# Optimization experiments

Hardware: AMD Instinct MI355X
Metric: run time of the kernel (lower is better)

## Reference

```python
import jax, jax.numpy as jnp
import numpy as np
import math

B, S, D, H, F, L, V = 16, 256, 1024, 16, 4096, 6, 32
HD = D // H
EPS = 1e-6
DIST_DECAY = 0.05  # grid-distance attention decay strength
NEG = -1e9


def _ln(x, w, b):
    mu = jnp.mean(x, axis=-1, keepdims=True)
    var = jnp.mean(jnp.square(x - mu), axis=-1, keepdims=True)
    return (x - mu) * jax.lax.rsqrt(var + EPS) * w + b


def _branch_bias():
    # branch 0: grid-distance decay (distance_matrix = |i-j|)
    # branch 1: register-flow edges i<->i+1 (chain mask)
    # branch 2: entanglement edges on even pairs (2k, 2k+1)
    # branch 3: semantic (full attention, no bias)
    i = jnp.arange(S)
    dist = jnp.abs(i[:, None] - i[None, :]).astype(jnp.float32)  # [S,S]
    reg = dist <= 1.0
    ent = (i[:, None] // 2) == (i[None, :] // 2)
    bias = jnp.stack([
        -DIST_DECAY * dist,
        jnp.where(reg, 0.0, NEG),
        jnp.where(ent, 0.0, NEG),
        jnp.zeros((S, S), jnp.float32),
    ])  # [4,S,S]
    return bias[:, None, None]  # [4,1,1,S,S]


def setup_inputs() -> dict:
    key = jax.random.key(0)
    ks = jax.random.split(key, 20)
    sd = 0.02
    inp = {
        'x': jax.random.normal(ks[0], (B, S, D), jnp.float32),
        't_emb': jax.random.normal(ks[1], (B, D), jnp.float32),
        'ln1_w': jnp.ones((L, D)), 'ln1_b': jnp.zeros((L, D)),
        'ln2_w': jnp.ones((L, D)), 'ln2_b': jnp.zeros((L, D)),
        'Wqkv': jax.random.normal(ks[2], (L, 4, D, 3 * D)) * sd,
        'Wo':   jax.random.normal(ks[3], (L, 4, D, D)) * sd,
        'Wf':   jax.random.normal(ks[4], (L, 4 * D, D)) * sd,
        'bf':   jnp.zeros((L, D)),
        'W1':   jax.random.normal(ks[5], (L, D, F)) * sd,
        'W3':   jax.random.normal(ks[6], (L, D, F)) * sd,
        'W2':   jax.random.normal(ks[7], (L, F, D)) * sd,
        'Wa':   jax.random.normal(ks[8], (L, D, 6 * D)) * sd,
        'ba':   jnp.zeros((L, 6 * D)),
        'fn_w': jnp.ones((D,)), 'fn_b': jnp.zeros((D,)),
        'Wp':   jax.random.normal(ks[9], (D, V)) * sd,
        'bp':   jnp.zeros((V,)),
    }
    return inp


def _quantum_attention(xn, Wqkv_l, Wo_l, Wf_l, bf_l, bias):
    # four attention branches computed in one batched einsum over branch axis x
    qkv = jnp.einsum('bsd,xde->xbse', xn, Wqkv_l)            # [4,B,S,3D]
    qkv = qkv.reshape(4, B, S, 3, H, HD)
    q, k, v = (jnp.moveaxis(qkv[:, :, :, j], 3, 2) for j in range(3))  # [4,B,H,S,HD]
    scores = jnp.einsum('xbhsd,xbhtd->xbhst', q, k) / math.sqrt(HD) + bias
    attn = jax.nn.softmax(scores, axis=-1)
    ctx = jnp.einsum('xbhst,xbhtd->xbhsd', attn, v)          # [4,B,H,S,HD]
    ctx = jnp.moveaxis(ctx, 2, 3).reshape(4, B, S, D)
    outs = jnp.einsum('xbsd,xde->xbse', ctx, Wo_l)           # [4,B,S,D]
    cat = jnp.moveaxis(outs, 0, 2).reshape(B, S, 4 * D)
    return cat @ Wf_l + bf_l                                  # fusion network


def reference(x, t_emb, ln1_w, ln1_b, ln2_w, ln2_b, Wqkv, Wo, Wf, bf, W1, W3, W2, Wa, ba, fn_w, fn_b, Wp, bp):
    bias = _branch_bias()
    for l in range(L):
        # AdaLN timestep conditioning: SiLU -> Linear -> chunk(6)
        a = jax.nn.silu(t_emb) @ Wa[l] + ba[l]
        sh_msa, sc_msa, g_msa, sh_mlp, sc_mlp, g_mlp = jnp.split(a, 6, axis=-1)
        xn = _ln(x, ln1_w[l], ln1_b[l])
        xn = xn * (1.0 + sc_msa[:, None]) + sh_msa[:, None]
        attn_out = _quantum_attention(xn, Wqkv[l], Wo[l], Wf[l], bf[l], bias)
        x = x + g_msa[:, None] * attn_out
        xn = _ln(x, ln2_w[l], ln2_b[l])
        xn = xn * (1.0 + sc_mlp[:, None]) + sh_mlp[:, None]
        ffn = (jax.nn.silu(xn @ W1[l]) * (xn @ W3[l])) @ W2[l]  # SwiGLU
        x = x + g_mlp[:, None] * ffn
    x = _ln(x, fn_w, fn_b)
    return x @ Wp + bp  # noise predictor logits [B,S,V]
```

## Files before the change

kernel.cpp:

```cpp
#include <hip/hip_runtime.h>
#include <hip/hip_bf16.h>
#include <math.h>

#define BB 16
#define SS 256
#define DD 1024
#define HH 16
#define HDD 64
#define FF 4096
#define LL 6
#define VV 32
#define MM (BB*SS)

using bf16 = __hip_bfloat16;
using short8 = __attribute__((ext_vector_type(8))) short;
using f32x4  = __attribute__((ext_vector_type(4))) float;

__device__ __forceinline__ float bf2f(short u){
  unsigned int x = ((unsigned int)(unsigned short)u) << 16;
  return __builtin_bit_cast(float, x);
}
__device__ __forceinline__ short f2bf(float f){
  return __builtin_bit_cast(short, __float2bfloat16(f));
}

__device__ __forceinline__ void gll16(const void* g, void* l) {
  __builtin_amdgcn_global_load_lds(
      (const __attribute__((address_space(1))) void*)g,
      (__attribute__((address_space(3))) void*)l,
      16, 0, 0);
}

__device__ __forceinline__ f32x4 mfma16(short8 a, short8 b, f32x4 c){
  return __builtin_amdgcn_mfma_f32_16x16x32_bf16(a, b, c, 0, 0, 0);
}

__device__ __forceinline__ void st_out(float* p, float v){ *p = v; }
__device__ __forceinline__ void st_out(bf16* p, float v){ *p = __float2bfloat16(v); }

__global__ __launch_bounds__(256)
void tcvt64(const float* __restrict__ in, bf16* __restrict__ out,
            int R, int C, long izs, long ozs)
{
  in  += (long)blockIdx.z * izs;
  out += (long)blockIdx.z * ozs;
  __shared__ float tl[64][65];
  int c0 = blockIdx.x * 64, r0 = blockIdx.y * 64;
  int t = threadIdx.x;
  int tr = t >> 4, tc = (t & 15) * 4;
  #pragma unroll
  for (int i = 0; i < 4; ++i) {
    f32x4 v = *(const f32x4*)(in + (long)(r0 + tr + i*16) * C + c0 + tc);
    tl[tr + i*16][tc+0] = v[0];
    tl[tr + i*16][tc+1] = v[1];
    tl[tr + i*16][tc+2] = v[2];
    tl[tr + i*16][tc+3] = v[3];
  }
  __syncthreads();
  int oc = t >> 2, rch = (t & 3) * 16;
  short8 o0, o1;
  #pragma unroll
  for (int j = 0; j < 8; ++j) o0[j] = f2bf(tl[rch + j][oc]);
  #pragma unroll
  for (int j = 0; j < 8; ++j) o1[j] = f2bf(tl[rch + 8 + j][oc]);
  *(short8*)(out + (long)(c0 + oc) * R + r0 + rch)     = o0;
  *(short8*)(out + (long)(c0 + oc) * R + r0 + rch + 8) = o1;
}

__global__ __launch_bounds__(256)
void tcvt64_w13(const float* __restrict__ W1, const float* __restrict__ W3,
                bf16* __restrict__ out, long loff)
{
  const float* in = (blockIdx.z ? W3 : W1) + loff;
  const int zoff = blockIdx.z ? 16 : 0;
  __shared__ float tl[64][65];
  int c0 = blockIdx.x * 64, r0 = blockIdx.y * 64;
  int t = threadIdx.x;
  int tr = t >> 4, tc = (t & 15) * 4;
  #pragma unroll
  for (int i = 0; i < 4; ++i) {
    f32x4 v = *(const f32x4*)(in + (long)(r0 + tr + i*16) * 4096 + c0 + tc);
    tl[tr + i*16][tc+0] = v[0];
    tl[tr + i*16][tc+1] = v[1];
    tl[tr + i*16][tc+2] = v[2];
    tl[tr + i*16][tc+3] = v[3];
  }
  __syncthreads();
  int oc = t >> 2, rch = (t & 3) * 16;
  short8 o0, o1;
  #pragma unroll
  for (int j = 0; j < 8; ++j) o0[j] = f2bf(tl[rch + j][oc]);
  #pragma unroll
  for (int j = 0; j < 8; ++j) o1[j] = f2bf(tl[rch + 8 + j][oc]);
  int n = c0 + oc;
  int orow = ((n >> 4) << 5) + zoff + (n & 15);
  *(short8*)(out + (long)orow * 1024 + r0 + rch)     = o0;
  *(short8*)(out + (long)orow * 1024 + r0 + rch + 8) = o1;
}

__global__ __launch_bounds__(256)
void cvt(const float* __restrict__ in, bf16* __restrict__ out)
{
  long base = ((long)blockIdx.x * 256 + threadIdx.x) * 8;
  f32x4 a = *(const f32x4*)(in + base);
  f32x4 b = *(const f32x4*)(in + base + 4);
  short8 o;
  #pragma unroll
  for (int j = 0; j < 4; ++j) { o[j] = f2bf(a[j]); o[4+j] = f2bf(b[j]); }
  *(short8*)(out + base) = o;
}

template<typename OUT, int MODE>
__global__ __launch_bounds__(512, 2)
void gemm256(const bf16* __restrict__ A, const bf16* __restrict__ Bt,
             OUT* __restrict__ C, int K,
             int lda, int ldb, int ldc, long kzs, long czs, int swz)
{
  __shared__ short lds[65536];
  char* L = (char*)lds;
  A  += (long)blockIdx.z * kzs;
  Bt += (long)blockIdx.z * kzs;
  C  += (long)blockIdx.z * czs;
  int lin = blockIdx.x + gridDim.x * blockIdx.y;
  if (swz) {
    int nwg = gridDim.x * gridDim.y;
    int q = nwg >> 3, r = nwg & 7;
    int xcd = lin & 7, o = lin >> 3;
    lin = (xcd < r ? xcd*(q+1) : r*(q+1) + (xcd-r)*q) + o;
  }
  const int n0 = (lin % gridDim.x) * 256;
  const int m0 = (lin / gridDim.x) * 256;
  const int t = threadIdx.x;
  const int wid = t >> 6, lane = t & 63, lo = lane & 15, hi = lane >> 4;
  const int wr = wid >> 2, wc = wid & 3;
  const int rst = t >> 3;
  const int glog = (t & 7) ^ (rst & 7);
  const int wub = wid * 1024;
  const bf16* Ap = A + (long)m0 * lda + glog * 8;
  const bf16* Bp = Bt + (long)n0 * ldb + glog * 8;
  f32x4 acc[8][4] = {};
  const int nkt = K >> 6;

  auto STAGE = [&](int kt, int p, int d) {
    const long ko = (long)kt * 64;
    char* base = L + d*65536;
    if (p < 2) {
      gll16(Ap + (long)((p*2  )*64 + rst)*lda + ko, base + (p*2  )*8192 + wub);
      gll16(Ap + (long)((p*2+1)*64 + rst)*lda + ko, base + (p*2+1)*8192 + wub);
    } else {
      int pp = p - 2;
      gll16(Bp + (long)((pp*2  )*64 + rst)*ldb + ko, base + 32768 + (pp*2  )*8192 + wub);
      gll16(Bp + (long)((pp*2+1)*64 + rst)*ldb + ko, base + 32768 + (pp*2+1)*8192 + wub);
    }
  };

  #pragma unroll
  for (int p = 0; p < 4; ++p) STAGE(0, p, 0);

  short8 af[4][2], b0[2][2], b1[2][2];
  const int gk0 = ((0*4 + hi) ^ (lo & 7)) << 4;
  const int gk1 = ((1*4 + hi) ^ (lo & 7)) << 4;

  for (int kt = 0; kt < nkt; ++kt) {
    const int d = kt & 1;
    const int ktn = (kt+1 < nkt) ? kt+1 : kt;
    char* Ab = L + d*65536;
    char* Bb = Ab + 32768;
    STAGE(ktn, 0, d^1);
    __builtin_amdgcn_sched_barrier(0);
    asm volatile("s_waitcnt vmcnt(2)" ::: "memory");
    __builtin_amdgcn_sched_barrier(0);
    __builtin_amdgcn_s_barrier();
    __builtin_amdgcn_sched_barrier(0);
    #pragma unroll
    for (int mi = 0; mi < 4; ++mi) {
      int r = wr*128 + mi*16 + lo;
      af[mi][0] = *(const short8*)(Ab + r*128 + gk0);
      af[mi][1] = *(const short8*)(Ab + r*128 + gk1);
    }
    #pragma unroll
    for (int ni = 0; ni < 2; ++ni) {
      int r = wc*64 + ni*16 + lo;
      b0[ni][0] = *(const short8*)(Bb + r*128 + gk0);
      b0[ni][1] = *(const short8*)(Bb + r*128 + gk1);
    }
    __builtin_amdgcn_s_barrier();
    __builtin_amdgcn_s_setprio(1);
    #pragma unroll
    for (int mi = 0; mi < 4; ++mi)
      #pragma unroll
      for (int ni = 0; ni < 2; ++ni) {
        acc[mi][ni] = mfma16(af[mi][0], b0[ni][0], acc[mi][ni]);
        acc[mi][ni] = mfma16(af[mi][1], b0[ni][1], acc[mi][ni]);
      }
    __builtin_amdgcn_s_setprio(0);
    __builtin_amdgcn_sched_barrier(0);
    __builtin_amdgcn_s_barrier();
    STAGE(ktn, 1, d^1);
    #pragma unroll
    for (int ni = 0; ni < 2; ++ni) {
      int r = wc*64 + (2+ni)*16 + lo;
      b1[ni][0] = *(const short8*)(Bb + r*128 + gk0);
      b1[ni][1] = *(const short8*)(Bb + r*128 + gk1);
    }
    __builtin_amdgcn_s_barrier();
    __builtin_amdgcn_s_setprio(1);
    #pragma unroll
    for (int mi = 0; mi < 4; ++mi)
      #pragma unroll
      for (int ni = 0; ni < 2; ++ni) {
        acc[mi][2+ni] = mfma16(af[mi][0], b1[ni][0], acc[mi][2+ni]);
        acc[mi][2+ni] = mfma16(af[mi][1], b1[ni][1], acc[mi][2+ni]);
      }
    __builtin_amdgcn_s_setprio(0);
    __builtin_amdgcn_sched_barrier(0);
    __builtin_amdgcn_s_barrier();
    STAGE(ktn, 2, d^1);
    #pragma unroll
    for (int mi = 0; mi < 4; ++mi) {
      int r = wr*128 + (4+mi)*16 + lo;
      af[mi][0] = *(const short8*)(Ab + r*128 + gk0);
      af[mi][1] = *(const short8*)(Ab + r*128 + gk1);
    }
    __builtin_amdgcn_s_barrier();
    __builtin_amdgcn_s_setprio(1);
    #pragma unroll
    for (int mi = 0; mi < 4; ++mi)
      #pragma unroll
      for (int ni = 0; ni < 2; ++ni) {
        acc[4+mi][2+ni] = mfma16(af[mi][0], b1[ni][0], acc[4+mi][2+ni]);
        acc[4+mi][2+ni] = mfma16(af[mi][1], b1[ni][1], acc[4+mi][2+ni]);
      }
    __builtin_amdgcn_s_setprio(0);
    __builtin_amdgcn_sched_barrier(0);
    __builtin_amdgcn_s_barrier();
    STAGE(ktn, 3, d^1);
    __builtin_amdgcn_s_barrier();
    __builtin_amdgcn_s_setprio(1);
    #pragma unroll
    for (int mi = 0; mi < 4; ++mi)
      #pragma unroll
      for (int ni = 0; ni < 2; ++ni) {
        acc[4+mi][ni] = mfma16(af[mi][0], b0[ni][0], acc[4+mi][ni]);
        acc[4+mi][ni] = mfma16(af[mi][1], b0[ni][1], acc[4+mi][ni]);
      }
    __builtin_amdgcn_s_setprio(0);
    __builtin_amdgcn_sched_barrier(0);
    __builtin_amdgcn_s_barrier();
  }
  if (MODE == 0) {
    #pragma unroll
    for (int mi = 0; mi < 8; ++mi)
      #pragma unroll
      for (int ni = 0; ni < 4; ++ni)
        #pragma unroll
        for (int r = 0; r < 4; ++r) {
          int row = m0 + wr*128 + mi*16 + hi*4 + r;
          int col = n0 + wc*64 + ni*16 + lo;
          st_out(C + (long)row * ldc + col, acc[mi][ni][r]);
        }
  } else {
    #pragma unroll
    for (int mi = 0; mi < 8; ++mi)
      #pragma unroll
      for (int k = 0; k < 2; ++k)
        #pragma unroll
        for (int r = 0; r < 4; ++r) {
          float h1 = acc[mi][2*k][r], h3 = acc[mi][2*k+1][r];
          float sv = h1 / (1.f + __expf(-h1)) * h3;
          int row = m0 + wr*128 + mi*16 + hi*4 + r;
          int col = (n0 >> 1) + wc*32 + k*16 + lo;
          st_out(C + (long)row * ldc + col, sv);
        }
  }
}

template<typename OUT>
__global__ __launch_bounds__(256)
void gemm_bt(const bf16* __restrict__ A, const bf16* __restrict__ Bt,
             OUT* __restrict__ C, int M, int N, int K,
             int lda, int ldb, int ldc,
             long azs, long bzs, long czs, int swz)
{
  const int z = blockIdx.z;
  A  += (long)z * azs;
  Bt += (long)z * bzs;
  C  += (long)z * czs;
  int bx = blockIdx.x, by = blockIdx.y;
  if (swz) {
    int nwg = gridDim.x * gridDim.y;
    int lin = bx + gridDim.x * by;
    int lin2 = (lin & 7) * (nwg >> 3) + (lin >> 3);
    bx = lin2 % gridDim.x;
    by = lin2 / gridDim.x;
  }
  const int n0 = bx * 128;
  const int m0 = by * 128;
  __shared__ short As[128*64];
  __shared__ short Bs[128*64];
  char* AsB = (char*)As;
  char* BsB = (char*)Bs;
  const int t = threadIdx.x;
  const int wid = t >> 6, lane = t & 63, lo = lane & 15, hi = lane >> 4;
  const int wr = wid >> 1, wc = wid & 1;
  const int rst  = t >> 3;
  const int glog = (t & 7) ^ (rst & 7);
  const int ldsbase = wid * 1024;
  f32x4 acc[4][4] = {};
  const bf16* Ap = A + (long)m0 * lda + glog * 8;
  const bf16* Bp = Bt + (long)n0 * ldb + glog * 8;
  const int nkt = K >> 6;
  for (int kt = 0; kt < nkt; ++kt) {
    const long ko = (long)kt * 64;
    #pragma unroll
    for (int i = 0; i < 4; ++i)
      gll16(Ap + (long)(i*32 + rst) * lda + ko, AsB + i*4096 + ldsbase);
    #pragma unroll
    for (int i = 0; i < 4; ++i)
      gll16(Bp + (long)(i*32 + rst) * ldb + ko, BsB + i*4096 + ldsbase);
    __syncthreads();
    #pragma unroll
    for (int kk = 0; kk < 2; ++kk) {
      const int g = ((kk*4 + hi) ^ (lo & 7)) << 4;
      short8 af[4], bfv[4];
      #pragma unroll
      for (int mi = 0; mi < 4; ++mi) {
        int r = wr*64 + mi*16 + lo;
        af[mi] = *(const short8*)(AsB + r*128 + g);
      }
      #pragma unroll
      for (int ni = 0; ni < 4; ++ni) {
        int r = wc*64 + ni*16 + lo;
        bfv[ni] = *(const short8*)(BsB + r*128 + g);
      }
      #pragma unroll
      for (int mi = 0; mi < 4; ++mi)
        #pragma unroll
        for (int ni = 0; ni < 4; ++ni)
          acc[mi][ni] = mfma16(af[mi], bfv[ni], acc[mi][ni]);
    }
    __syncthreads();
  }
  #pragma unroll
  for (int mi = 0; mi < 4; ++mi)
    #pragma unroll
    for (int ni = 0; ni < 4; ++ni)
      #pragma unroll
      for (int r = 0; r < 4; ++r) {
        int row = m0 + wr*64 + mi*16 + hi*4 + r;
        int col = n0 + wc*64 + ni*16 + lo;
        st_out(C + (long)row * ldc + col, acc[mi][ni][r]);
      }
}

__global__ __launch_bounds__(256)
void vtk(const bf16* __restrict__ qkv, bf16* __restrict__ vt)
{
  int xbh = blockIdx.y;
  int xc = xbh >> 8, b = (xbh >> 4) & 15, h = xbh & 15;
  int x = xc * 3;
  int tch = blockIdx.x;
  const unsigned short* src = (const unsigned short*)qkv
      + (long)(b*SS + tch*64) * 12288 + x*3072 + 2048 + h*64;
  unsigned short* dst = (unsigned short*)vt + (long)xbh * 64 * 256 + tch*64;
  __shared__ unsigned short tl[64][66];
  int t = threadIdx.x;
  #pragma unroll
  for (int i = 0; i < 16; ++i) {
    int idx = t + i*256; int tt = idx >> 6, dd = idx & 63;
    tl[tt][dd] = src[(long)tt * 12288 + dd];
  }
  __syncthreads();
  #pragma unroll
  for (int i = 0; i < 16; ++i) {
    int idx = t + i*256; int dd = idx >> 6, t2 = idx & 63;
    dst[(long)dd * 256 + t2] = tl[t2][dd];
  }
}

__device__ __forceinline__ float bias_f(int x, int i, int j){
  if (x == 0) { int d = i > j ? i - j : j - i; return -0.05f * (float)d; }
  return 0.f;
}

__global__ __launch_bounds__(256)
void attn_k(const bf16* __restrict__ qkv, const bf16* __restrict__ vt,
            bf16* __restrict__ ctx)
{
  const int xc = blockIdx.y;
  const int x = xc * 3;
  const int bh = blockIdx.x;
  const int b = bh >> 4, h = bh & 15;
  const int t = threadIdx.x, wid = t >> 6, lane = t & 63;
  const int lo = lane & 15, hi = lane >> 4;
  const int q0 = wid * 64;
  __shared__ short Pl[4][64*64];
  char* P = (char*)Pl[wid];
  const bf16* qb = qkv + (long)(b*SS) * 12288 + x*3072 + h*64;
  const bf16* kb = qb + 1024;
  const bf16* vb = vt + (long)(xc*256 + b*16 + h) * 64 * 256;

  short8 qf[4][2];
  #pragma unroll
  for (int mi = 0; mi < 4; ++mi)
    #pragma unroll
    for (int kk = 0; kk < 2; ++kk)
      qf[mi][kk] = *(const short8*)(qb + (long)(q0 + mi*16 + lo) * 12288 + kk*32 + hi*8);

  float mr[4][4], sr[4][4];
  f32x4 aco[4][4] = {};
  #pragma unroll
  for (int i = 0; i < 4; ++i)
    #pragma unroll
    for (int r = 0; r < 4; ++r) { mr[i][r] = -INFINITY; sr[i][r] = 0.f; }

  for (int c = 0; c < 4; ++c) {
    f32x4 acc[4][4] = {};
    #pragma unroll
    for (int kk = 0; kk < 2; ++kk) {
      short8 bfv[4];
      #pragma unroll
      for (int ni = 0; ni < 4; ++ni)
        bfv[ni] = *(const short8*)(kb + (long)(c*64 + ni*16 + lo) * 12288 + kk*32 + hi*8);
      #pragma unroll
      for (int mi = 0; mi < 4; ++mi)
        #pragma unroll
        for (int ni = 0; ni < 4; ++ni)
          acc[mi][ni] = mfma16(qf[mi][kk], bfv[ni], acc[mi][ni]);
    }
    float cmax[4][4];
    #pragma unroll
    for (int mi = 0; mi < 4; ++mi)
      #pragma unroll
      for (int r = 0; r < 4; ++r) cmax[mi][r] = -INFINITY;
    #pragma unroll
    for (int mi = 0; mi < 4; ++mi)
      #pragma unroll
      for (int ni = 0; ni < 4; ++ni)
        #pragma unroll
        for (int r = 0; r < 4; ++r) {
          int qq = q0 + mi*16 + hi*4 + r;
          int tt = c*64 + ni*16 + lo;
          float v = acc[mi][ni][r] * 0.125f + bias_f(x, qq, tt);
          acc[mi][ni][r] = v;
          cmax[mi][r] = fmaxf(cmax[mi][r], v);
        }
    #pragma unroll
    for (int mi = 0; mi < 4; ++mi)
      #pragma unroll
      for (int r = 0; r < 4; ++r) {
        float m = cmax[mi][r];
        #pragma unroll
        for (int d = 1; d < 16; d <<= 1) m = fmaxf(m, __shfl_xor(m, d));
        cmax[mi][r] = m;
      }
    float fs[4][4];
    #pragma unroll
    for (int mi = 0; mi < 4; ++mi)
      #pragma unroll
      for (int r = 0; r < 4; ++r) {
        float mo = mr[mi][r];
        float mn = fmaxf(mo, cmax[mi][r]);
        float f = __expf(mo - mn);
        mr[mi][r] = mn; sr[mi][r] *= f; fs[mi][r] = f;
      }
    #pragma unroll
    for (int mi = 0; mi < 4; ++mi)
      #pragma unroll
      for (int di = 0; di < 4; ++di)
        #pragma unroll
        for (int r = 0; r < 4; ++r) aco[mi][di][r] *= fs[mi][r];
    #pragma unroll
    for (int mi = 0; mi < 4; ++mi)
      #pragma unroll
      for (int ni = 0; ni < 4; ++ni)
        #pragma unroll
        for (int r = 0; r < 4; ++r) {
          int qq = mi*16 + hi*4 + r;
          float pv = __expf(acc[mi][ni][r] - mr[mi][r]);
          sr[mi][r] += pv;
          int tt = ni*16 + lo;
          int gph = ((tt >> 3) ^ (qq & 7)) << 4;
          *(bf16*)(P + qq*128 + gph + (tt & 7)*2) = __float2bfloat16(pv);
        }
    #pragma unroll
    for (int kk = 0; kk < 2; ++kk) {
      short8 pf[4], vf[4];
      #pragma unroll
      for (int mi = 0; mi < 4; ++mi) {
        int qq = mi*16 + lo;
        int gph = ((kk*4 + hi) ^ (qq & 7)) << 4;
        pf[mi] = *(const short8*)(P + qq*128 + gph);
      }
      #pragma unroll
      for (int di = 0; di < 4; ++di)
        vf[di] = *(const short8*)(vb + (long)(di*16 + lo) * 256 + c*64 + kk*32 + hi*8);
      #pragma unroll
      for (int mi = 0; mi < 4; ++mi)
        #pragma unroll
        for (int di = 0; di < 4; ++di)
          aco[mi][di] = mfma16(pf[mi], vf[di], aco[mi][di]);
    }
  }
  #pragma unroll
  for (int mi = 0; mi < 4; ++mi)
    #pragma unroll
    for (int r = 0; r < 4; ++r) {
      float s = sr[mi][r];
      #pragma unroll
      for (int d = 1; d < 16; d <<= 1) s += __shfl_xor(s, d);
      sr[mi][r] = s;
    }
  bf16* cb = ctx + (long)(b*SS) * 4096 + x*1024 + h*64;
  #pragma unroll
  for (int mi = 0; mi < 4; ++mi)
    #pragma unroll
    for (int di = 0; di < 4; ++di)
      #pragma unroll
      for (int r = 0; r < 4; ++r) {
        int row = q0 + mi*16 + hi*4 + r;
        int col = di*16 + lo;
        cb[(long)row * 4096 + col] = __float2bfloat16(aco[mi][di][r] / sr[mi][r]);
      }
}

__global__ __launch_bounds__(256)
void br12_k(const bf16* __restrict__ qkv, bf16* __restrict__ ctx)
{
  const unsigned short* Q = (const unsigned short*)qkv;
  const int wid = threadIdx.x >> 6, lane = threadIdx.x & 63;
  const int b = blockIdx.x >> 6, c = blockIdx.x & 63;
  const int i = c*4 + wid;
  const long rowQ = (long)(b*SS + i) * 12288;
  const long rb = (long)(b*SS) * 12288;
  const int jm = i > 0 ? i-1 : 0;
  const int jp = i < SS-1 ? i+1 : SS-1;
  const int j0 = i & ~1, j1 = j0 | 1;
  unsigned short* outp = (unsigned short*)ctx + (long)(b*SS + i) * 4096;
  for (int h = 0; h < HH; ++h) {
    const int off1 = 3072 + h*64 + lane;
    const int off2 = 6144 + h*64 + lane;
    float q1d = bf2f(Q[rowQ + off1]);
    float q2d = bf2f(Q[rowQ + off2]);
    float km = bf2f(Q[rb + (long)jm*12288 + off1 + 1024]);
    float k0 = bf2f(Q[rb + (long)i *12288 + off1 + 1024]);
    float kp = bf2f(Q[rb + (long)jp*12288 + off1 + 1024]);
    float ka = bf2f(Q[rb + (long)j0*12288 + off2 + 1024]);
    float kb_ = bf2f(Q[rb + (long)j1*12288 + off2 + 1024]);
    float s0 = q1d*km, s1 = q1d*k0, s2 = q1d*kp, s3 = q2d*ka, s4 = q2d*kb_;
    #pragma unroll
    for (int st = 1; st < 64; st <<= 1) {
      s0 += __shfl_xor(s0, st); s1 += __shfl_xor(s1, st); s2 += __shfl_xor(s2, st);
      s3 += __shfl_xor(s3, st); s4 += __shfl_xor(s4, st);
    }
    float lm = s0*0.125f + (i > 0      ? 0.f : -1e30f);
    float l0 = s1*0.125f;
    float lp = s2*0.125f + (i < SS-1   ? 0.f : -1e30f);
    float m1 = fmaxf(l0, fmaxf(lm, lp));
    float pm = __expf(lm-m1), p0 = __expf(l0-m1), pp = __expf(lp-m1);
    float vm = bf2f(Q[rb + (long)jm*12288 + off1 + 2048]);
    float v0 = bf2f(Q[rb + (long)i *12288 + off1 + 2048]);
    float vp = bf2f(Q[rb + (long)jp*12288 + off1 + 2048]);
    float o1 = (pm*vm + p0*v0 + pp*vp) / (pm+p0+pp);
    float la = s3*0.125f, lb = s4*0.125f;
    float m2 = fmaxf(la, lb);
    float pa = __expf(la-m2), pb = __expf(lb-m2);
    float va = bf2f(Q[rb + (long)j0*12288 + off2 + 2048]);
    float vb2= bf2f(Q[rb + (long)j1*12288 + off2 + 2048]);
    float o2 = (pa*va + pb*vb2) / (pa+pb);
    outp[1024 + h*64 + lane] = (unsigned short)f2bf(o1);
    outp[2048 + h*64 + lane] = (unsigned short)f2bf(o2);
  }
}

__global__ __launch_bounds__(256)
void ln_fused(const float* __restrict__ xin, const float* __restrict__ y,
              int ycnt, long ystride,
              const float* __restrict__ ybias, const float* __restrict__ gate,
              const float* __restrict__ lnw, const float* __restrict__ lnb,
              const float* __restrict__ sc, const float* __restrict__ sh,
              float* __restrict__ xout, bf16* __restrict__ xnbf,
              float* __restrict__ xnf)
{
  int row = blockIdx.x;
  int b = row >> 8;
  int t = threadIdx.x;
  int d0 = t * 4;
  const float* xr = xin + (long)row * DD;
  f32x4 xi = *(const f32x4*)(xr + d0);
  float v[4];
  if (y) {
    f32x4 ys = {};
    for (int jp = 0; jp < ycnt; ++jp) {
      f32x4 yi = *(const f32x4*)(y + jp*ystride + (long)row * DD + d0);
      #pragma unroll
      for (int j = 0; j < 4; ++j) ys[j] += yi[j];
    }
    #pragma unroll
    for (int j = 0; j < 4; ++j) {
      float yy = ys[j] + (ybias ? ybias[d0+j] : 0.f);
      v[j] = xi[j] + gate[b*6144 + d0 + j] * yy;
    }
  } else {
    #pragma unroll
    for (int j = 0; j < 4; ++j) v[j] = xi[j];
  }
  if (xout) {
    f32x4 o; o[0]=v[0]; o[1]=v[1]; o[2]=v[2]; o[3]=v[3];
    *(f32x4*)(xout + (long)row * DD + d0) = o;
  }
  float s = v[0]+v[1]+v[2]+v[3];
  float s2 = v[0]*v[0]+v[1]*v[1]+v[2]*v[2]+v[3]*v[3];
  #pragma unroll
  for (int d = 1; d < 64; d <<= 1) { s += __shfl_xor(s, d); s2 += __shfl_xor(s2, d); }
  __shared__ float rs[4][2];
  int wid = t >> 6, lane = t & 63;
  if (lane == 0) { rs[wid][0] = s; rs[wid][1] = s2; }
  __syncthreads();
  s  = rs[0][0]+rs[1][0]+rs[2][0]+rs[3][0];
  s2 = rs[0][1]+rs[1][1]+rs[2][1]+rs[3][1];
  float mean = s * (1.f/1024.f);
  float var  = s2 * (1.f/1024.f) - mean*mean;
  float rstd = rsqrtf(var + 1e-6f);
  #pragma unroll
  for (int j = 0; j < 4; ++j) {
    int d = d0 + j;
    float xn = (v[j] - mean) * rstd * lnw[d] + lnb[d];
    if (sc) {
      float val = xn * (1.f + sc[b*6144 + d]) + sh[b*6144 + d];
      xnbf[(long)row * DD + d] = __float2bfloat16(val);
    } else if (xnbf) {
      xnbf[(long)row * DD + d] = __float2bfloat16(xn);
    } else {
      xnf[(long)row * DD + d] = xn;
    }
  }
}

__global__ __launch_bounds__(256)
void silu_k(const float* __restrict__ te, float* __restrict__ st)
{
  int i = blockIdx.x * 256 + threadIdx.x;
  float v = te[i];
  st[i] = v / (1.f + __expf(-v));
}

__global__ __launch_bounds__(256)
void a_gemm(const float* __restrict__ Wa, const float* __restrict__ st,
            float* __restrict__ partial)
{
  int l = blockIdx.z, kc = blockIdx.y;
  int n0 = (blockIdx.x * 256 + threadIdx.x) * 4;
  __shared__ float sl[16*128];
  for (int i = threadIdx.x; i < 16*128; i += 256) {
    int m = i >> 7, k = i & 127;
    sl[i] = st[m*1024 + kc*128 + k];
  }
  __syncthreads();
  f32x4 acc[16] = {};
  const float* wp = Wa + (long)l * DD * 6144 + (long)(kc*128) * 6144 + n0;
  #pragma unroll 2
  for (int k = 0; k < 128; ++k) {
    f32x4 w = *(const f32x4*)(wp + (long)k * 6144);
    #pragma unroll
    for (int m = 0; m < 16; ++m) {
      float sv = sl[m*128 + k];
      #pragma unroll
      for (int j = 0; j < 4; ++j) acc[m][j] += sv * w[j];
    }
  }
  #pragma unroll
  for (int m = 0; m < 16; ++m)
    *(f32x4*)(partial + ((long)(l*8 + kc)*16 + m) * 6144 + n0) = acc[m];
}

__global__ __launch_bounds__(256)
void a_red(const float* __restrict__ partial, const float* __restrict__ ba,
           float* __restrict__ a_all)
{
  int idx = blockIdx.x * 256 + threadIdx.x;
  int n = idx % 6144;
  int lm = idx / 6144;
  int l = lm >> 4, m = lm & 15;
  float s = 0.f;
  #pragma unroll
  for (int kc = 0; kc < 8; ++kc)
    s += partial[((long)(l*8 + kc)*16 + m) * 6144 + n];
  a_all[(long)(l*16 + m) * 6144 + n] = s + ba[(long)l * 6144 + n];
}

__global__ __launch_bounds__(256)
void proj_k(const float* __restrict__ xnf, const float* __restrict__ Wp,
            const float* __restrict__ bp, float* __restrict__ out)
{
  int v = threadIdx.x & 31, tg = threadIdx.x >> 5;
  int s = blockIdx.x * 8 + tg;
  const float* xr = xnf + (long)s * DD;
  float acc = bp[v];
  #pragma unroll 8
  for (int k = 0; k < DD; ++k) acc += xr[k] * Wp[(long)k * VV + v];
  out[(long)s * VV + v] = acc;
}

extern "C" void kernel_launch(void* const* d_in, const int* in_sizes, int n_in,
                              void* d_out, int out_size, void* d_ws, size_t ws_size,
                              hipStream_t stream)
{
  (void)in_sizes; (void)n_in; (void)out_size; (void)ws_size;
  const float* x_in = (const float*)d_in[0];
  const float* t_emb= (const float*)d_in[1];
  const float* ln1w = (const float*)d_in[2];
  const float* ln1b = (const float*)d_in[3];
  const float* ln2w = (const float*)d_in[4];
  const float* ln2b = (const float*)d_in[5];
  const float* Wqkv = (const float*)d_in[6];
  const float* Wo   = (const float*)d_in[7];
  const float* Wf   = (const float*)d_in[8];
  const float* bfb  = (const float*)d_in[9];
  const float* W1   = (const float*)d_in[10];
  const float* W3   = (const float*)d_in[11];
  const float* W2   = (const float*)d_in[12];
  const float* Wa   = (const float*)d_in[13];
  const float* ba   = (const float*)d_in[14];
  const float* fnw  = (const float*)d_in[15];
  const float* fnb  = (const float*)d_in[16];
  const float* Wp   = (const float*)d_in[17];
  const float* bp   = (const float*)d_in[18];
  float* out = (float*)d_out;

  char* p = (char*)d_ws;
  auto alloc = [&](size_t bytes) { char* r = p; p += (bytes + 255) & ~(size_t)255; return r; };
  bf16* wqkv_t = (bf16*)alloc(4L*3072*1024*2);
  bf16* wo_b   = (bf16*)alloc(4L*1024*1024*2);
  bf16* wf_t   = (bf16*)alloc(1024L*4096*2);
  bf16* wof_t  = (bf16*)alloc(1024L*4096*2);
  bf16* w13i_t = (bf16*)alloc(8192L*1024*2);
  bf16* w2_t   = (bf16*)alloc(1024L*4096*2);
  float* a_all = (float*)alloc(6L*16*6144*4);
  float* a_par = (float*)alloc(6L*8*16*6144*4);
  float* st    = (float*)alloc(16L*1024*4);
  float* x_buf = (float*)alloc((long)MM*DD*4);
  bf16* xn     = (bf16*)alloc((long)MM*DD*2);
  char* bufA   = alloc((long)MM*12288*2);
  bf16* vt     = (bf16*)alloc(2L*16*16*64*256*2);
  bf16* ctx    = (bf16*)alloc((long)MM*4096*2);
  char* bufB   = alloc((long)MM*4096*2);
  float* gy    = (float*)alloc(4L*MM*DD*4);

  bf16* qkvb = (bf16*)bufA;
  bf16* hg   = (bf16*)bufB;
  float* xnf = (float*)bufB;
  const long MMDD = (long)MM*DD;

  silu_k<<<dim3(64), 256, 0, stream>>>(t_emb, st);
  a_gemm<<<dim3(6, 8, 6), 256, 0, stream>>>(Wa, st, a_par);
  a_red<<<dim3(2304), 256, 0, stream>>>(a_par, ba, a_all);

  const long aL = 16L * 6144;
  for (int l = 0; l < LL; ++l) {
    const float* a_l = a_all + (long)l * aL;
    tcvt64<<<dim3(48,16,4),256,0,stream>>>(Wqkv + (long)l*4*1024*3072, wqkv_t, 1024, 3072, 1024L*3072, 3072L*1024);
    cvt<<<dim3(2048),256,0,stream>>>(Wo + (long)l*4*1024*1024, wo_b);
    tcvt64<<<dim3(16,64,1),256,0,stream>>>(Wf  + (long)l*4096*1024,  wf_t,   4096, 1024, 0, 0);
    tcvt64_w13<<<dim3(64,16,2),256,0,stream>>>(W1, W3, w13i_t, (long)l*1024*4096);
    tcvt64<<<dim3(16,64,1),256,0,stream>>>(W2  + (long)l*4096*1024,  w2_t,   4096, 1024, 0, 0);
    gemm_bt<bf16><<<dim3(8,8,4),256,0,stream>>>(wf_t, wo_b, wof_t,
        1024, 1024, 1024, 4096, 1024, 4096, 1024L, 1024L*1024, 1024L, 0);

    if (l == 0)
      ln_fused<<<4096,256,0,stream>>>(x_in, nullptr, 0, 0, nullptr, nullptr,
                                      ln1w, ln1b, a_l+1024, a_l+0,
                                      nullptr, xn, nullptr);

    gemm256<bf16,0><<<dim3(48,16,1),512,0,stream>>>(xn, wqkv_t, qkvb,
        1024, 1024, 1024, 12288, 0, 0, 1);
    vtk<<<dim3(4,512),256,0,stream>>>(qkvb, vt);
    attn_k<<<dim3(256,2),256,0,stream>>>(qkvb, vt, ctx);
    br12_k<<<dim3(1024),256,0,stream>>>(qkvb, ctx);
    gemm256<float,0><<<dim3(4,16,4),512,0,stream>>>(ctx, wof_t, gy,
        1024, 4096, 4096, 1024, 1024L, MMDD, 0);
    ln_fused<<<4096,256,0,stream>>>(l ? x_buf : x_in, gy, 4, MMDD,
                                    bfb + (long)l*1024, a_l+2048,
                                    ln2w + (long)l*1024, ln2b + (long)l*1024,
                                    a_l+4096, a_l+3072, x_buf, xn, nullptr);
    gemm256<bf16,1><<<dim3(32,16,1),512,0,stream>>>(xn, w13i_t, hg,
        1024, 1024, 1024, 4096, 0, 0, 1);
    gemm256<float,0><<<dim3(4,16,4),512,0,stream>>>(hg, w2_t, gy,
        1024, 4096, 4096, 1024, 1024L, MMDD, 0);
    if (l < LL-1)
      ln_fused<<<4096,256,0,stream>>>(x_buf, gy, 4, MMDD, nullptr, a_l+5120,
                                      ln1w + (long)(l+1)*1024, ln1b + (long)(l+1)*1024,
                                      a_all + (long)(l+1)*aL + 1024, a_all + (long)(l+1)*aL,
                                      x_buf, xn, nullptr);
    else
      ln_fused<<<4096,256,0,stream>>>(x_buf, gy, 4, MMDD, nullptr, a_l+5120,
                                      fnw, fnb, nullptr, nullptr,
                                      x_buf, nullptr, xnf);
  }
  proj_k<<<dim3(512),256,0,stream>>>(xnf, Wp, bp, out);
}
```

Before: 3.009 ms.

## Batch all-layer weight conversion upfront, fuse V transpose into QKV GEMM epilogue

```diff
diff --git a/kernel.cpp b/kernel.cpp
--- a/kernel.cpp
+++ b/kernel.cpp
@@ -13,6 +13,7 @@
 #define MM (BB*SS)
 
 using bf16 = __hip_bfloat16;
+using short4v = __attribute__((ext_vector_type(4))) short;
 using short8 = __attribute__((ext_vector_type(8))) short;
 using f32x4  = __attribute__((ext_vector_type(4))) float;
 
@@ -69,10 +70,12 @@
 
 __global__ __launch_bounds__(256)
 void tcvt64_w13(const float* __restrict__ W1, const float* __restrict__ W3,
-                bf16* __restrict__ out, long loff)
-{
-  const float* in = (blockIdx.z ? W3 : W1) + loff;
-  const int zoff = blockIdx.z ? 16 : 0;
+                bf16* __restrict__ out)
+{
+  int l = blockIdx.z >> 1;
+  const float* in = ((blockIdx.z & 1) ? W3 : W1) + (long)l * 1024 * 4096;
+  const int zoff = (blockIdx.z & 1) ? 16 : 0;
+  bf16* o = out + (long)l * 8192 * 1024;
   __shared__ float tl[64][65];
   int c0 = blockIdx.x * 64, r0 = blockIdx.y * 64;
   int t = threadIdx.x;
@@ -94,8 +97,8 @@
   for (int j = 0; j < 8; ++j) o1[j] = f2bf(tl[rch + 8 + j][oc]);
   int n = c0 + oc;
   int orow = ((n >> 4) << 5) + zoff + (n & 15);
-  *(short8*)(out + (long)orow * 1024 + r0 + rch)     = o0;
-  *(short8*)(out + (long)orow * 1024 + r0 + rch + 8) = o1;
+  *(short8*)(o + (long)orow * 1024 + r0 + rch)     = o0;
+  *(short8*)(o + (long)orow * 1024 + r0 + rch + 8) = o1;
 }
 
 __global__ __launch_bounds__(256)
@@ -114,7 +117,8 @@
 __global__ __launch_bounds__(512, 2)
 void gemm256(const bf16* __restrict__ A, const bf16* __restrict__ Bt,
              OUT* __restrict__ C, int K,
-             int lda, int ldb, int ldc, long kzs, long czs, int swz)
+             int lda, int ldb, int ldc, long kzs, long czs, int swz,
+             bf16* __restrict__ vtp)
 {
   __shared__ short lds[65536];
   char* L = (char*)lds;
@@ -248,18 +252,7 @@
     __builtin_amdgcn_sched_barrier(0);
     __builtin_amdgcn_s_barrier();
   }
-  if (MODE == 0) {
-    #pragma unroll
-    for (int mi = 0; mi < 8; ++mi)
-      #pragma unroll
-      for (int ni = 0; ni < 4; ++ni)
-        #pragma unroll
-        for (int r = 0; r < 4; ++r) {
-          int row = m0 + wr*128 + mi*16 + hi*4 + r;
-          int col = n0 + wc*64 + ni*16 + lo;
-          st_out(C + (long)row * ldc + col, acc[mi][ni][r]);
-        }
-  } else {
+  if (MODE == 1) {
     #pragma unroll
     for (int mi = 0; mi < 8; ++mi)
       #pragma unroll
@@ -272,7 +265,39 @@
           int col = (n0 >> 1) + wc*32 + k*16 + lo;
           st_out(C + (long)row * ldc + col, sv);
         }
-  }
+    return;
+  }
+  if (MODE == 2) {
+    int xt = n0 / 3072, rem = n0 - xt*3072;
+    if (rem >= 2048 && (xt == 0 || xt == 3)) {
+      const int xc = xt ? 1 : 0;
+      const int b = m0 >> 8;
+      #pragma unroll
+      for (int mi = 0; mi < 8; ++mi)
+        #pragma unroll
+        for (int ni = 0; ni < 4; ++ni) {
+          int col = n0 + wc*64 + ni*16 + lo;
+          int hd = col - xt*3072 - 2048;
+          int h = hd >> 6, dd = hd & 63;
+          int trow = wr*128 + mi*16 + hi*4;
+          short4v pk;
+          #pragma unroll
+          for (int r = 0; r < 4; ++r) pk[r] = f2bf(acc[mi][ni][r]);
+          *(short4v*)(vtp + ((long)((xc<<8)+(b<<4)+h)*64 + dd)*256 + trow) = pk;
+        }
+      return;
+    }
+  }
+  #pragma unroll
+  for (int mi = 0; mi < 8; ++mi)
+    #pragma unroll
+    for (int ni = 0; ni < 4; ++ni)
+      #pragma unroll
+      for (int r = 0; r < 4; ++r) {
+        int row = m0 + wr*128 + mi*16 + hi*4 + r;
+        int col = n0 + wc*64 + ni*16 + lo;
+        st_out(C + (long)row * ldc + col, acc[mi][ni][r]);
+      }
 }
 
 template<typename OUT>
@@ -280,22 +305,15 @@
 void gemm_bt(const bf16* __restrict__ A, const bf16* __restrict__ Bt,
              OUT* __restrict__ C, int M, int N, int K,
              int lda, int ldb, int ldc,
-             long azs, long bzs, long czs, int swz)
-{
-  const int z = blockIdx.z;
-  A  += (long)z * azs;
-  Bt += (long)z * bzs;
-  C  += (long)z * czs;
-  int bx = blockIdx.x, by = blockIdx.y;
-  if (swz) {
-    int nwg = gridDim.x * gridDim.y;
-    int lin = bx + gridDim.x * by;
-    int lin2 = (lin & 7) * (nwg >> 3) + (lin >> 3);
-    bx = lin2 % gridDim.x;
-    by = lin2 / gridDim.x;
-  }
-  const int n0 = bx * 128;
-  const int m0 = by * 128;
+             long azs, long bzs, long czs, int zdiv,
+             long azs2, long bzs2, long czs2)
+{
+  const int z1 = blockIdx.z % zdiv, z2 = blockIdx.z / zdiv;
+  A  += (long)z1 * azs + (long)z2 * azs2;
+  Bt += (long)z1 * bzs + (long)z2 * bzs2;
+  C  += (long)z1 * czs + (long)z2 * czs2;
+  const int n0 = blockIdx.x * 128;
+  const int m0 = blockIdx.y * 128;
   __shared__ short As[128*64];
   __shared__ short Bs[128*64];
   char* AsB = (char*)As;
@@ -353,31 +371,6 @@
       }
 }
 
-__global__ __launch_bounds__(256)
-void vtk(const bf16* __restrict__ qkv, bf16* __restrict__ vt)
-{
-  int xbh = blockIdx.y;
-  int xc = xbh >> 8, b = (xbh >> 4) & 15, h = xbh & 15;
-  int x = xc * 3;
-  int tch = blockIdx.x;
-  const unsigned short* src = (const unsigned short*)qkv
-      + (long)(b*SS + tch*64) * 12288 + x*3072 + 2048 + h*64;
-  unsigned short* dst = (unsigned short*)vt + (long)xbh * 64 * 256 + tch*64;
-  __shared__ unsigned short tl[64][66];
-  int t = threadIdx.x;
-  #pragma unroll
-  for (int i = 0; i < 16; ++i) {
-    int idx = t + i*256; int tt = idx >> 6, dd = idx & 63;
-    tl[tt][dd] = src[(long)tt * 12288 + dd];
-  }
-  __syncthreads();
-  #pragma unroll
-  for (int i = 0; i < 16; ++i) {
-    int idx = t + i*256; int dd = idx >> 6, t2 = idx & 63;
-    dst[(long)dd * 256 + t2] = tl[t2][dd];
-  }
-}
-
 __device__ __forceinline__ float bias_f(int x, int i, int j){
   if (x == 0) { int d = i > j ? i - j : j - i; return -0.05f * (float)d; }
   return 0.f;
@@ -529,15 +522,16 @@
 {
   const unsigned short* Q = (const unsigned short*)qkv;
   const int wid = threadIdx.x >> 6, lane = threadIdx.x & 63;
-  const int b = blockIdx.x >> 6, c = blockIdx.x & 63;
-  const int i = c*4 + wid;
+  const int b = blockIdx.x >> 8, i = blockIdx.x & 255;
   const long rowQ = (long)(b*SS + i) * 12288;
   const long rb = (long)(b*SS) * 12288;
   const int jm = i > 0 ? i-1 : 0;
   const int jp = i < SS-1 ? i+1 : SS-1;
   const int j0 = i & ~1, j1 = j0 | 1;
   unsigned short* outp = (unsigned short*)ctx + (long)(b*SS + i) * 4096;
-  for (int h = 0; h < HH; ++h) {
+  #pragma unroll
+  for (int hh = 0; hh < 4; ++hh) {
+    const int h = wid*4 + hh;
     const int off1 = 3072 + h*64 + lane;
     const int off2 = 6144 + h*64 + lane;
     float q1d = bf2f(Q[rowQ + off1]);
@@ -730,12 +724,12 @@
 
   char* p = (char*)d_ws;
   auto alloc = [&](size_t bytes) { char* r = p; p += (bytes + 255) & ~(size_t)255; return r; };
-  bf16* wqkv_t = (bf16*)alloc(4L*3072*1024*2);
-  bf16* wo_b   = (bf16*)alloc(4L*1024*1024*2);
-  bf16* wf_t   = (bf16*)alloc(1024L*4096*2);
-  bf16* wof_t  = (bf16*)alloc(1024L*4096*2);
-  bf16* w13i_t = (bf16*)alloc(8192L*1024*2);
-  bf16* w2_t   = (bf16*)alloc(1024L*4096*2);
+  bf16* wqkv_t = (bf16*)alloc(6L*4*3072*1024*2);
+  bf16* wo_b   = (bf16*)alloc(6L*4*1024*1024*2);
+  bf16* wf_t   = (bf16*)alloc(6L*1024*4096*2);
+  bf16* wof_t  = (bf16*)alloc(6L*1024*4096*2);
+  bf16* w13i_t = (bf16*)alloc(6L*8192*1024*2);
+  bf16* w2_t   = (bf16*)alloc(6L*1024*4096*2);
   float* a_all = (float*)alloc(6L*16*6144*4);
   float* a_par = (float*)alloc(6L*8*16*6144*4);
   float* st    = (float*)alloc(16L*1024*4);
@@ -755,38 +749,37 @@
   silu_k<<<dim3(64), 256, 0, stream>>>(t_emb, st);
   a_gemm<<<dim3(6, 8, 6), 256, 0, stream>>>(Wa, st, a_par);
   a_red<<<dim3(2304), 256, 0, stream>>>(a_par, ba, a_all);
+  tcvt64<<<dim3(48,16,24),256,0,stream>>>(Wqkv, wqkv_t, 1024, 3072, 1024L*3072, 3072L*1024);
+  cvt<<<dim3(12288),256,0,stream>>>(Wo, wo_b);
+  tcvt64<<<dim3(16,64,6),256,0,stream>>>(Wf, wf_t, 4096, 1024, 4096L*1024, 4096L*1024);
+  tcvt64_w13<<<dim3(64,16,12),256,0,stream>>>(W1, W3, w13i_t);
+  tcvt64<<<dim3(16,64,6),256,0,stream>>>(W2, w2_t, 4096, 1024, 4096L*1024, 4096L*1024);
+  gemm_bt<bf16><<<dim3(8,8,24),256,0,stream>>>(wf_t, wo_b, wof_t,
+      1024, 1024, 1024, 4096, 1024, 4096,
+      1024L, 1024L*1024, 1024L, 4,
+      1024L*4096, 4L*1024*1024, 1024L*4096);
 
   const long aL = 16L * 6144;
+  ln_fused<<<4096,256,0,stream>>>(x_in, nullptr, 0, 0, nullptr, nullptr,
+                                  ln1w, ln1b, a_all+1024, a_all+0,
+                                  nullptr, xn, nullptr);
+
   for (int l = 0; l < LL; ++l) {
     const float* a_l = a_all + (long)l * aL;
-    tcvt64<<<dim3(48,16,4),256,0,stream>>>(Wqkv + (long)l*4*1024*3072, wqkv_t, 1024, 3072, 1024L*3072, 3072L*1024);
-    cvt<<<dim3(2048),256,0,stream>>>(Wo + (long)l*4*1024*1024, wo_b);
-    tcvt64<<<dim3(16,64,1),256,0,stream>>>(Wf  + (long)l*4096*1024,  wf_t,   4096, 1024, 0, 0);
-    tcvt64_w13<<<dim3(64,16,2),256,0,stream>>>(W1, W3, w13i_t, (long)l*1024*4096);
-    tcvt64<<<dim3(16,64,1),256,0,stream>>>(W2  + (long)l*4096*1024,  w2_t,   4096, 1024, 0, 0);
-    gemm_bt<bf16><<<dim3(8,8,4),256,0,stream>>>(wf_t, wo_b, wof_t,
-        1024, 1024, 1024, 4096, 1024, 4096, 1024L, 1024L*1024, 1024L, 0);
-
-    if (l == 0)
-      ln_fused<<<4096,256,0,stream>>>(x_in, nullptr, 0, 0, nullptr, nullptr,
-                                      ln1w, ln1b, a_l+1024, a_l+0,
-                                      nullptr, xn, nullptr);
-
-    gemm256<bf16,0><<<dim3(48,16,1),512,0,stream>>>(xn, wqkv_t, qkvb,
-        1024, 1024, 1024, 12288, 0, 0, 1);
-    vtk<<<dim3(4,512),256,0,stream>>>(qkvb, vt);
+    gemm256<bf16,2><<<dim3(48,16,1),512,0,stream>>>(xn, wqkv_t + (long)l*4*3072*1024,
+        qkvb, 1024, 1024, 1024, 12288, 0, 0, 1, vt);
     attn_k<<<dim3(256,2),256,0,stream>>>(qkvb, vt, ctx);
-    br12_k<<<dim3(1024),256,0,stream>>>(qkvb, ctx);
-    gemm256<float,0><<<dim3(4,16,4),512,0,stream>>>(ctx, wof_t, gy,
-        1024, 4096, 4096, 1024, 1024L, MMDD, 0);
+    br12_k<<<dim3(4096),256,0,stream>>>(qkvb, ctx);
+    gemm256<float,0><<<dim3(4,16,4),512,0,stream>>>(ctx, wof_t + (long)l*1024*4096,
+        gy, 1024, 4096, 4096, 1024, 1024L, MMDD, 0, nullptr);
     ln_fused<<<4096,256,0,stream>>>(l ? x_buf : x_in, gy, 4, MMDD,
                                     bfb + (long)l*1024, a_l+2048,
                                     ln2w + (long)l*1024, ln2b + (long)l*1024,
                                     a_l+4096, a_l+3072, x_buf, xn, nullptr);
-    gemm256<bf16,1><<<dim3(32,16,1),512,0,stream>>>(xn, w13i_t, hg,
-        1024, 1024, 1024, 4096, 0, 0, 1);
-    gemm256<float,0><<<dim3(4,16,4),512,0,stream>>>(hg, w2_t, gy,
-        1024, 4096, 4096, 1024, 1024L, MMDD, 0);
+    gemm256<bf16,1><<<dim3(32,16,1),512,0,stream>>>(xn, w13i_t + (long)l*8192*1024,
+        hg, 1024, 1024, 1024, 4096, 0, 0, 1, nullptr);
+    gemm256<float,0><<<dim3(4,16,4),512,0,stream>>>(hg, w2_t + (long)l*1024*4096,
+        gy, 1024, 4096, 4096, 1024, 1024L, MMDD, 0, nullptr);
     if (l < LL-1)
       ln_fused<<<4096,256,0,stream>>>(x_buf, gy, 4, MMDD, nullptr, a_l+5120,
                                       ln1w + (long)(l+1)*1024, ln1b + (long)(l+1)*1024,
```

Result: faster. 2.939 ms (-2.4%).
